# Kernel tuning notes

Measured on AMD Instinct MI355X. Metric: run time of the kernel, lower is better.

The kernel has to match this reference:

```python
import jax, jax.numpy as jnp
import numpy as np

NEG_SLOPE = 0.2  # PyG GATConv default leaky_relu slope
BN_EPS = 1e-5


def gat_conv(x_src, x_dst, src, dst, w_src, w_dst, att_src, att_dst, bias):
    """Bipartite PyG GATConv, heads=H, concat=False (mean over heads), add_self_loops=True.
    x_src: [Ns, F], x_dst: [Nd, F]; src/dst: [E] int edge index; w_*: [F, H*C]; att_*: [H, C]; bias: [C].
    """
    H, C = att_src.shape
    n_dst = x_dst.shape[0]
    hs = (x_src @ w_src).reshape(-1, H, C)            # [Ns, H, C]
    hd = (x_dst @ w_dst).reshape(-1, H, C)            # [Nd, H, C]
    a_s = (hs * att_src[None]).sum(-1)                # [Ns, H]
    a_d = (hd * att_dst[None]).sum(-1)                # [Nd, H]
    # PyG adds self loops with num_nodes = min(Ns, Nd) for bipartite inputs
    n_loop = min(x_src.shape[0], n_dst)
    loop = jnp.arange(n_loop, dtype=src.dtype)
    src = jnp.concatenate([src, loop])
    dst = jnp.concatenate([dst, loop])
    e = jax.nn.leaky_relu(a_s[src] + a_d[dst], NEG_SLOPE)           # [E+L, H]
    m = jax.ops.segment_max(e, dst, num_segments=n_dst)             # [Nd, H]
    ex = jnp.exp(e - m[dst])
    den = jax.ops.segment_sum(ex, dst, num_segments=n_dst)
    alpha = ex / (den[dst] + 1e-16)                                 # neighborhood softmax
    msg = hs[src] * alpha[:, :, None]                               # [E+L, H, C]
    out = jax.ops.segment_sum(msg, dst, num_segments=n_dst)         # [Nd, H, C]
    return out.mean(axis=1) + bias


def _forward(user_ids, ingredient_ids, recipe_x, ing_src, ing_dst, ub_src, ub_dst,
             user_table, ing_table, W_rl, b_rl, bn_gamma, bn_beta,
             g1_ws, g1_wd, g1_as, g1_ad, g1_b,
             g2_ws, g2_wd, g2_as, g2_ad, g2_b):
    # nn.Embedding(max_norm=1.0): renorm looked-up rows to L2 norm <= 1
    u = user_table[user_ids]
    un = jnp.linalg.norm(u, axis=-1, keepdims=True)
    u = u * jnp.where(un > 1.0, 1.0 / (un + 1e-7), 1.0)
    # static ingredient embedding lookup
    ing = ing_table[ingredient_ids]
    # recipe linear + BatchNorm (training-mode batch stats; dropout off = eval)
    r = recipe_x @ W_rl + b_rl
    mu = r.mean(axis=0)
    var = ((r - mu) ** 2).mean(axis=0)
    r = bn_gamma * (r - mu) * jax.lax.rsqrt(var + BN_EPS) + bn_beta
    # ingredient -> recipe GAT, residual add
    r = r + gat_conv(ing, r, ing_src, ing_dst, g1_ws, g1_wd, g1_as, g1_ad, g1_b)
    # user -> recipe GAT
    r = gat_conv(u, r, ub_src, ub_dst, g2_ws, g2_wd, g2_as, g2_ad, g2_b)
    return r


def setup_inputs() -> dict:
    key = jax.random.key(0)
    ks = jax.random.split(key, 24)
    NU, NR, NI = 50000, 100000, 20000
    D_IN, H, C = 20, 2, 128
    E1, E2 = 400000, 800000
    s = 0.05
    f32 = jnp.float32
    inp = {
        "user_ids": jax.random.randint(ks[0], (NU,), 0, NU, dtype=jnp.int32),
        "ingredient_ids": jax.random.randint(ks[1], (NI,), 0, NI, dtype=jnp.int32),
        "recipe_x": jax.random.normal(ks[2], (NR, D_IN), f32),
        "ing_src": jax.random.randint(ks[3], (E1,), 0, NI, dtype=jnp.int32),
        "ing_dst": jax.random.randint(ks[4], (E1,), 0, NR, dtype=jnp.int32),
        "ub_src": jax.random.randint(ks[5], (E2,), 0, NU, dtype=jnp.int32),
        "ub_dst": jax.random.randint(ks[6], (E2,), 0, NR, dtype=jnp.int32),
        "user_table": jax.random.normal(ks[7], (NU, C), f32) * s,
        "ing_table": jax.random.normal(ks[8], (NI, C), f32) * s,
        "W_rl": jax.random.normal(ks[9], (D_IN, C), f32) * s,
        "b_rl": jnp.zeros((C,), f32),
        "bn_gamma": jnp.ones((C,), f32),
        "bn_beta": jnp.zeros((C,), f32),
        "g1_ws": jax.random.normal(ks[10], (C, H * C), f32) * s,
        "g1_wd": jax.random.normal(ks[11], (C, H * C), f32) * s,
        "g1_as": jax.random.normal(ks[12], (H, C), f32) * s,
        "g1_ad": jax.random.normal(ks[13], (H, C), f32) * s,
        "g1_b": jnp.zeros((C,), f32),
        "g2_ws": jax.random.normal(ks[14], (C, H * C), f32) * s,
        "g2_wd": jax.random.normal(ks[15], (C, H * C), f32) * s,
        "g2_as": jax.random.normal(ks[16], (H, C), f32) * s,
        "g2_ad": jax.random.normal(ks[17], (H, C), f32) * s,
        "g2_b": jnp.zeros((C,), f32),
    }
    return inp


def reference(user_ids, ingredient_ids, recipe_x, ing_src, ing_dst, ub_src, ub_dst,
              user_table, ing_table, W_rl, b_rl, bn_gamma, bn_beta,
              g1_ws, g1_wd, g1_as, g1_ad, g1_b,
              g2_ws, g2_wd, g2_as, g2_ad, g2_b):
    return _forward(user_ids, ingredient_ids, recipe_x, ing_src, ing_dst, ub_src, ub_dst,
                    user_table, ing_table, W_rl, b_rl, bn_gamma, bn_beta,
                    g1_ws, g1_wd, g1_as, g1_ad, g1_b,
                    g2_ws, g2_wd, g2_as, g2_ad, g2_b)
```

## Files before the change

kernel.cpp:

```cpp
#include <hip/hip_runtime.h>
#include <hip/hip_bf16.h>
#include <math.h>

#define DIN 20
#define C 128
#define HC 256
#define EB2 1024
#define MAXNB 400
#define CAP 8192
#define CAPSH 13

typedef unsigned short u16;
typedef unsigned int u32;
typedef unsigned long long u64;
typedef __bf16 bf16x8 __attribute__((ext_vector_type(8)));
typedef float f32x4 __attribute__((ext_vector_type(4)));

__device__ __forceinline__ float bfbits2f(unsigned int lo16) {
    return __uint_as_float(lo16 << 16);
}
__device__ __forceinline__ u16 f2bf_rne(float f) {
    unsigned int b = __float_as_uint(f);
    return (u16)((b + 0x7FFFu + ((b >> 16) & 1u)) >> 16);
}

__device__ __forceinline__ void scan512f(u32* cnt, u32* off, u32* wsum4) {
    int t = threadIdx.x;
    int l = t & 63, w = t >> 6;
    u32 a = cnt[2 * t], b = cnt[2 * t + 1];
    u32 s = a + b;
    u32 isc = s;
    #pragma unroll
    for (int o = 1; o < 64; o <<= 1) {
        u32 n = __shfl_up(isc, o);
        if (l >= o) isc += n;
    }
    if (l == 63) wsum4[w] = isc;
    __syncthreads();
    u32 pre = 0;
    if (w > 0) pre += wsum4[0];
    if (w > 1) pre += wsum4[1];
    if (w > 2) pre += wsum4[2];
    u32 excl = pre + isc - s;
    off[2 * t] = excl;
    off[2 * t + 1] = excl + a;
    __syncthreads();
}

__device__ __forceinline__ void edge_at(int i, const int* s1, const int* d1,
    const int* s2, const int* d2, int E1, int T1, int E2, int NR,
    int& s, int& key)
{
    if (i < T1) {
        if (i < E1) { s = s1[i]; key = d1[i]; }
        else        { s = i - E1; key = i - E1; }
    } else {
        int k = i - T1;
        if (k < E2) { s = s2[k]; key = NR + d2[k]; }
        else        { s = k - E2; key = NR + (k - E2); }
    }
}

__global__ __launch_bounds__(256) void k_init(const float* __restrict__ x, int NR,
    float* __restrict__ stats, int SB, int A2B,
    const int* __restrict__ src1, const int* __restrict__ dst1,
    const int* __restrict__ src2, const int* __restrict__ dst2,
    int E1, int L1, int E2, int L2, int NB,
    u32* __restrict__ bucketFill, u64* __restrict__ pairs,
    const float* __restrict__ g2_ws, u16* __restrict__ wsp)
{
    __shared__ __align__(16) char sm[24144];
    int t = threadIdx.x;
    int bid = blockIdx.x;
    if (bid < SB) {
        float (*L)[DIN] = (float(*)[DIN])sm;
        int r = bid * 256 + t;
        if (r < NR) {
            #pragma unroll
            for (int k = 0; k < DIN; k++) L[t][k] = x[r * DIN + k];
        } else {
            #pragma unroll
            for (int k = 0; k < DIN; k++) L[t][k] = 0.f;
        }
        __syncthreads();
        if (t < 210) {
            int p = 0, q = t;
            while (q >= DIN - p) { q -= (DIN - p); p++; }
            q += p;
            float acc = 0.f;
            for (int rr = 0; rr < 256; rr++) acc += L[rr][p] * L[rr][q];
            atomicAdd(&stats[p * DIN + q], acc);
            if (p != q) atomicAdd(&stats[q * DIN + p], acc);
        } else if (t < 230) {
            int k = t - 210;
            float acc = 0.f;
            for (int rr = 0; rr < 256; rr++) acc += L[rr][k];
            atomicAdd(&stats[400 + k], acc);
        }
        return;
    }
    if (bid < SB + A2B) {
        u64* ldsE = (u64*)sm;
        u64* ldsS = ldsE + EB2;
        u32* cntA = (u32*)(ldsS + EB2);
        u32* cntB = cntA + 512;
        u32* offL = cntB + 512;
        u32* wsum4 = offL + 512;
        u32* gbase = wsum4 + 4;
        for (int i = t; i < 512; i += 256) { cntA[i] = 0; cntB[i] = 0; }
        __syncthreads();
        int T1 = E1 + L1, T = T1 + E2 + L2;
        int base = (bid - SB) * EB2;
        int nE = T - base; if (nE > EB2) nE = EB2;
        for (int j = t; j < nE; j += 256) {
            int s, key;
            edge_at(base + j, src1, dst1, src2, dst2, E1, T1, E2, NR, s, key);
            ldsE[j] = ((u64)(u32)key << 32) | (u32)s;
            atomicAdd(&cntA[key >> 9], 1u);
        }
        __syncthreads();
        scan512f(cntA, offL, wsum4);
        for (int b = t; b < NB; b += 256) {
            u32 c = cntA[b];
            gbase[b] = c ? (((u32)b << CAPSH) + atomicAdd(&bucketFill[b], c)) : 0u;
        }
        __syncthreads();
        for (int j = t; j < nE; j += 256) {
            u64 e = ldsE[j];
            u32 b = ((u32)(e >> 32)) >> 9;
            u32 r = atomicAdd(&cntB[b], 1u);
            ldsS[offL[b] + r] = e;
        }
        __syncthreads();
        for (int j = t; j < nE; j += 256) {
            u64 e = ldsS[j];
            u32 b = ((u32)(e >> 32)) >> 9;
            pairs[gbase[b] + ((u32)j - offL[b])] = e;
        }
        return;
    }
    int idx0 = ((bid - SB - A2B) * 256 + t) * 4;
    #pragma unroll
    for (int i = 0; i < 4; i++) {
        int flat = idx0 + i;
        int j = flat & 7;
        int lane = (flat >> 3) & 63;
        int kb = (flat >> 9) & 3;
        int nt = flat >> 11;
        int k = kb * 32 + (lane >> 4) * 8 + j;
        int n = nt * 16 + (lane & 15);
        wsp[flat] = f2bf_rne(g2_ws[k * HC + n]);
    }
}

__global__ __launch_bounds__(256) void k_pre(float* __restrict__ stats,
    const float* __restrict__ W,
    const float* __restrict__ gamma, const float* __restrict__ beta,
    const float* __restrict__ g1_wd, const float* __restrict__ g1_ad,
    const float* __restrict__ g2_wd, const float* __restrict__ g2_ad,
    const float* __restrict__ g1_ws, const float* __restrict__ g1_as,
    const float* __restrict__ g2_ws, const float* __restrict__ g2_as,
    const float* __restrict__ g1b, float invN)
{
    int t = threadIdx.x;
    __shared__ float Sm[420];
    __shared__ float Wm[DIN * C];
    __shared__ float vd1s[256];
    __shared__ float vd2s[256];
    __shared__ float sS[128];
    __shared__ float sSh[128];
    for (int i = t; i < 420; i += 256) Sm[i] = stats[i];
    for (int i = t; i < DIN * C; i += 256) Wm[i] = W[i];
    __syncthreads();
    if (t < C) {
        float w[DIN];
        #pragma unroll
        for (int k = 0; k < DIN; k++) w[k] = Wm[k * C + t];
        float mb = 0.f;
        #pragma unroll
        for (int k = 0; k < DIN; k++) mb += Sm[400 + k] * invN * w[k];
        float e2 = 0.f;
        for (int p = 0; p < DIN; p++) {
            float acc2 = 0.f;
            #pragma unroll
            for (int q = 0; q < DIN; q++) acc2 += Sm[p * DIN + q] * w[q];
            e2 += w[p] * acc2;
        }
        e2 *= invN;
        float var = e2 - mb * mb;
        float s = gamma[t] * rsqrtf(var + 1e-5f);
        float sh = beta[t] - s * mb;
        stats[420 + t] = s;
        stats[548 + t] = sh;
        sS[t] = s;
        sSh[t] = sh;
    }
    {
        int k = t >> 1, h = t & 1;
        const float4* wd1 = (const float4*)(g1_wd + k * HC + h * C);
        const float4* wd2 = (const float4*)(g2_wd + k * HC + h * C);
        const float4* ws1 = (const float4*)(g1_ws + k * HC + h * C);
        const float4* ws2 = (const float4*)(g2_ws + k * HC + h * C);
        const float4* ad1 = (const float4*)(g1_ad + h * C);
        const float4* ad2 = (const float4*)(g2_ad + h * C);
        const float4* as1 = (const float4*)(g1_as + h * C);
        const float4* as2 = (const float4*)(g2_as + h * C);
        float a1 = 0.f, a2 = 0.f, s1 = 0.f, s2 = 0.f;
        #pragma unroll 4
        for (int q = 0; q < 32; q++) {
            float4 x, y;
            x = wd1[q]; y = ad1[q];
            a1 += x.x * y.x + x.y * y.y + x.z * y.z + x.w * y.w;
            x = wd2[q]; y = ad2[q];
            a2 += x.x * y.x + x.y * y.y + x.z * y.z + x.w * y.w;
            x = ws1[q]; y = as1[q];
            s1 += x.x * y.x + x.y * y.y + x.z * y.z + x.w * y.w;
            x = ws2[q]; y = as2[q];
            s2 += x.x * y.x + x.y * y.y + x.z * y.z + x.w * y.w;
        }
        stats[676 + t] = a1;
        stats[932 + t] = a2;
        stats[1200 + t] = s1;
        stats[1456 + t] = s2;
        vd1s[t] = a1;
        vd2s[t] = a2;
    }
    __syncthreads();
    {
        int k = t >> 1, h = t & 1;
        const float4* ws1p = (const float4*)(g1_ws + k * HC + h * C);
        float t0 = 0.f, t1 = 0.f;
        #pragma unroll 4
        for (int q = 0; q < 32; q++) {
            float4 wv = ws1p[q];
            int c = q * 4;
            t0 += wv.x * vd2s[(c + 0) * 2 + 0] + wv.y * vd2s[(c + 1) * 2 + 0]
                + wv.z * vd2s[(c + 2) * 2 + 0] + wv.w * vd2s[(c + 3) * 2 + 0];
            t1 += wv.x * vd2s[(c + 0) * 2 + 1] + wv.y * vd2s[(c + 1) * 2 + 1]
                + wv.z * vd2s[(c + 2) * 2 + 1] + wv.w * vd2s[(c + 3) * 2 + 1];
        }
        stats[1712 + t * 2 + 0] = t0;
        stats[1712 + t * 2 + 1] = t1;
    }
    if (t < 2) {
        float cb = 0.f;
        for (int k = 0; k < C; k++) cb += g1b[k] * vd2s[k * 2 + t];
        stats[1188 + t] = cb;
    }
    if (t < 80) {
        int k = t >> 2, h4 = t & 3, h = h4 & 1;
        const float* vs = (h4 < 2) ? vd1s : vd2s;
        float acc = 0.f;
        for (int c = 0; c < C; c++) acc += sS[c] * Wm[k * C + c] * vs[c * 2 + h];
        stats[2240 + t] = acc;
    } else if (t < 84) {
        int h4 = t - 80, h = h4 & 1;
        const float* vs = (h4 < 2) ? vd1s : vd2s;
        float acc = 0.f;
        for (int c = 0; c < C; c++) acc += sSh[c] * vs[c * 2 + h];
        stats[2320 + h4] = acc;
    }
}

__global__ __launch_bounds__(256) void k_fin(const u64* __restrict__ pairs,
    const u32* __restrict__ bucketFill, int n2, int NB, int R0B, int IB,
    int* __restrict__ off2, int* __restrict__ sorted,
    const float* __restrict__ x, int NR, const float* __restrict__ stats,
    float* __restrict__ a_d, float* __restrict__ advd,
    const float* __restrict__ ing_table, const int* __restrict__ ing_ids, int NI,
    float* __restrict__ a_si, float* __restrict__ psi,
    const float* __restrict__ user_table, const int* __restrict__ user_ids, int NU,
    const u16* __restrict__ wsp, u16* __restrict__ hs16, float* __restrict__ a_su)
{
    __shared__ __align__(16) char sm[30736];
    int t = threadIdx.x;
    int bid = blockIdx.x;
    if (bid < NB) {
        u32* cntA = (u32*)sm;
        u32* cntB = cntA + 512;
        u32* offL = cntB + 512;
        u32* wsum4 = offL + 512;
        u32* ldsS = wsum4 + 4;
        int b = bid;
        u32 beg = (u32)b << CAPSH;
        u32 fill = bucketFill[b];
        u32 end = beg + fill;
        int dstBase = b << 9;
        for (int i = t; i < 512; i += 256) { cntA[i] = 0; cntB[i] = 0; }
        __syncthreads();
        for (u32 j = beg + t; j < end; j += 256) {
            u32 key = (u32)(pairs[j] >> 32);
            atomicAdd(&cntA[key - dstBase], 1u);
        }
        __syncthreads();
        scan512f(cntA, offL, wsum4);
        for (int d = t; d < 512; d += 256) {
            int gk = dstBase + d;
            if (gk < n2) {
                int s0 = (int)(beg + offL[d]);
                off2[2 * gk] = s0;
                off2[2 * gk + 1] = s0 + (int)cntA[d];
            }
        }
        bool fast = fill <= 6144u;
        __syncthreads();
        for (u32 j = beg + t; j < end; j += 256) {
            u64 e = pairs[j];
            u32 d = (u32)(e >> 32) - dstBase;
            u32 r = atomicAdd(&cntB[d], 1u);
            u32 pos = offL[d] + r;
            if (fast) ldsS[pos] = (u32)e;
            else sorted[beg + pos] = (int)(u32)e;
        }
        __syncthreads();
        if (fast) {
            for (u32 j = t; j < fill; j += 256) sorted[beg + j] = (int)ldsS[j];
        }
        return;
    }
    if (bid < NB + R0B) {
        float* fv = (float*)sm;
        if (t < 84) fv[t] = stats[2240 + t];
        __syncthreads();
        int r = (bid - NB) * 256 + t;
        if (r < NR) {
            const float4* xp = (const float4*)(x + (size_t)r * DIN);
            float4 v0 = xp[0], v1 = xp[1], v2 = xp[2], v3 = xp[3], v4 = xp[4];
            float xv[20] = {v0.x, v0.y, v0.z, v0.w, v1.x, v1.y, v1.z, v1.w,
                            v2.x, v2.y, v2.z, v2.w, v3.x, v3.y, v3.z, v3.w,
                            v4.x, v4.y, v4.z, v4.w};
            float a0 = 0.f, a1 = 0.f, b0 = 0.f, b1 = 0.f;
            #pragma unroll
            for (int k = 0; k < DIN; k++) {
                float xvk = xv[k];
                a0 += xvk * fv[k * 4 + 0];
                a1 += xvk * fv[k * 4 + 1];
                b0 += xvk * fv[k * 4 + 2];
                b1 += xvk * fv[k * 4 + 3];
            }
            ((float2*)a_d)[r]  = make_float2(a0 + fv[80], a1 + fv[81]);
            ((float2*)advd)[r] = make_float2(b0 + fv[82], b1 + fv[83]);
        }
        return;
    }
    if (bid < NB + R0B + IB) {
        float* u1s = (float*)sm;
        float* Ts  = u1s + 256;
        u1s[t] = stats[1200 + t];
        Ts[t] = stats[1712 + t];
        Ts[256 + t] = stats[1968 + t];
        __syncthreads();
        int r = t >> 3, cg = t & 7;
        int row = (bid - NB - R0B) * 32 + r;
        float as0 = 0.f, as1 = 0.f, p00 = 0.f, p01 = 0.f, p10 = 0.f, p11 = 0.f;
        if (row < NI) {
            const float* xp = ing_table + (size_t)ing_ids[row] * C + cg * 16;
            #pragma unroll
            for (int q = 0; q < 4; q++) {
                float4 v = ((const float4*)xp)[q];
                float xvv[4] = {v.x, v.y, v.z, v.w};
                #pragma unroll
                for (int jj = 0; jj < 4; jj++) {
                    int k = cg * 16 + q * 4 + jj;
                    float xx = xvv[jj];
                    as0 += xx * u1s[k * 2 + 0];
                    as1 += xx * u1s[k * 2 + 1];
                    p00 += xx * Ts[k * 4 + 0];
                    p01 += xx * Ts[k * 4 + 1];
                    p10 += xx * Ts[k * 4 + 2];
                    p11 += xx * Ts[k * 4 + 3];
                }
            }
        }
        #pragma unroll
        for (int m = 1; m <= 4; m <<= 1) {
            as0 += __shfl_xor(as0, m); as1 += __shfl_xor(as1, m);
            p00 += __shfl_xor(p00, m); p01 += __shfl_xor(p01, m);
            p10 += __shfl_xor(p10, m); p11 += __shfl_xor(p11, m);
        }
        if (cg == 0 && row < NI) {
            ((float2*)a_si)[row] = make_float2(as0, as1);
            float4 pv; pv.x = p00; pv.y = p01; pv.z = p10; pv.w = p11;
            ((float4*)psi)[row] = pv;
        }
        return;
    }
    u16* A = (u16*)sm;
    float* u2s = (float*)(sm + 8704);
    u2s[t] = stats[1456 + t];
    int rowBase = (bid - NB - R0B - IB) * 32;
    int r = t >> 3, cg = t & 7;
    int row = rowBase + r;
    float xv[16];
    if (row < NU) {
        const float* xp = user_table + (size_t)user_ids[row] * C + cg * 16;
        #pragma unroll
        for (int q = 0; q < 4; q++) {
            float4 v = ((const float4*)xp)[q];
            xv[q * 4 + 0] = v.x; xv[q * 4 + 1] = v.y;
            xv[q * 4 + 2] = v.z; xv[q * 4 + 3] = v.w;
        }
    } else {
        #pragma unroll
        for (int q = 0; q < 16; q++) xv[q] = 0.f;
    }
    float ss = 0.f;
    #pragma unroll
    for (int q = 0; q < 16; q++) ss += xv[q] * xv[q];
    #pragma unroll
    for (int m = 1; m <= 4; m <<= 1) ss += __shfl_xor(ss, m);
    float nn = sqrtf(ss);
    float f = (nn > 1.f) ? 1.f / (nn + 1e-7f) : 1.f;
    float as0 = 0.f, as1 = 0.f;
    #pragma unroll
    for (int q = 0; q < 16; q++) {
        xv[q] *= f;
        int k = cg * 16 + q;
        as0 += xv[q] * u2s[k * 2 + 0];
        as1 += xv[q] * u2s[k * 2 + 1];
    }
    #pragma unroll
    for (int m = 1; m <= 4; m <<= 1) {
        as0 += __shfl_xor(as0, m); as1 += __shfl_xor(as1, m);
    }
    if (cg == 0 && row < NU) ((float2*)a_su)[row] = make_float2(as0, as1);
    {
        union { u16 h[16]; uint4 u4[2]; } pk;
        #pragma unroll
        for (int q = 0; q < 16; q++) pk.h[q] = f2bf_rne(xv[q]);
        uint4* dst = (uint4*)&A[r * 136 + cg * 16];
        dst[0] = pk.u4[0];
        dst[1] = pk.u4[1];
    }
    __syncthreads();
    int w = t >> 6, l = t & 63;
    int m15 = l & 15, q4 = l >> 4;
    bf16x8 afrag[2][4];
    #pragma unroll
    for (int mt = 0; mt < 2; mt++)
        #pragma unroll
        for (int kb = 0; kb < 4; kb++)
            afrag[mt][kb] = *(const bf16x8*)&A[(mt * 16 + m15) * 136 + kb * 32 + q4 * 8];
    f32x4 acc[2][4];
    #pragma unroll
    for (int mt = 0; mt < 2; mt++)
        #pragma unroll
        for (int i = 0; i < 4; i++) acc[mt][i] = (f32x4){0.f, 0.f, 0.f, 0.f};
    #pragma unroll
    for (int kb = 0; kb < 4; kb++) {
        #pragma unroll
        for (int i = 0; i < 4; i++) {
            int nt = w * 4 + i;
            bf16x8 bfrag = *(const bf16x8*)&wsp[((nt * 4 + kb) * 64 + l) * 8];
            acc[0][i] = __builtin_amdgcn_mfma_f32_16x16x32_bf16(afrag[0][kb], bfrag, acc[0][i], 0, 0, 0);
            acc[1][i] = __builtin_amdgcn_mfma_f32_16x16x32_bf16(afrag[1][kb], bfrag, acc[1][i], 0, 0, 0);
        }
    }
    #pragma unroll
    for (int mt = 0; mt < 2; mt++) {
        #pragma unroll
        for (int i = 0; i < 4; i++) {
            int col = (w * 4 + i) * 16 + m15;
            #pragma unroll
            for (int rr = 0; rr < 4; rr++) {
                int rw = rowBase + mt * 16 + q4 * 4 + rr;
                if (rw < NU) hs16[(size_t)rw * HC + col] = f2bf_rne(acc[mt][i][rr]);
            }
        }
    }
}

__global__ __launch_bounds__(256) void k_agg(const int* __restrict__ off2, const int* __restrict__ sorted,
    const float* __restrict__ a_si, const float* __restrict__ psi,
    const float* __restrict__ a_d1, const float* __restrict__ advd,
    const float* __restrict__ cb,
    const float* __restrict__ a_su, const u16* __restrict__ hs16,
    const float* __restrict__ bias, int NR, float* __restrict__ out)
{
    int wave = threadIdx.x >> 6, lane = threadIdx.x & 63;
    int d = blockIdx.x * 4 + wave;
    if (d >= NR) return;
    int beg = off2[2 * d], end = off2[2 * d + 1];
    float ad0 = a_d1[d * 2 + 0], ad1 = a_d1[d * 2 + 1];
    float w0s = 0.f, w1s = 0.f, a00 = 0.f, a01 = 0.f, a10 = 0.f, a11 = 0.f;
    for (int j = beg + lane; j < end; j += 64) {
        int s = sorted[j];
        float2 as = ((const float2*)a_si)[s];
        float e0 = as.x + ad0; e0 = (e0 >= 0.f) ? e0 : 0.2f * e0;
        float e1 = as.y + ad1; e1 = (e1 >= 0.f) ? e1 : 0.2f * e1;
        float x0 = __expf(e0), x1 = __expf(e1);
        float4 p = ((const float4*)psi)[s];
        w0s += x0; w1s += x1;
        a00 += x0 * p.x; a01 += x0 * p.y;
        a10 += x1 * p.z; a11 += x1 * p.w;
    }
    #pragma unroll
    for (int o = 1; o < 64; o <<= 1) {
        w0s += __shfl_xor(w0s, o); w1s += __shfl_xor(w1s, o);
        a00 += __shfl_xor(a00, o); a01 += __shfl_xor(a01, o);
        a10 += __shfl_xor(a10, o); a11 += __shfl_xor(a11, o);
    }
    float inv0g = 1.f / (w0s + 1e-16f), inv1g = 1.f / (w1s + 1e-16f);
    float r0 = advd[d * 2 + 0] + cb[0] + 0.5f * (a00 * inv0g + a10 * inv1g);
    float r1 = advd[d * 2 + 1] + cb[1] + 0.5f * (a01 * inv0g + a11 * inv1g);
    int i2 = NR + d;
    int beg2 = off2[2 * i2], end2 = off2[2 * i2 + 1];
    int head = lane >> 5;
    int q = lane & 31;
    u32 laneoff = (u32)(head * 256 + q * 8);
    int hsel = lane & 32;
    float adh = head ? r1 : r0;
    float wsum = 0.f;
    float acc0 = 0.f, acc1 = 0.f, acc2 = 0.f, acc3 = 0.f;
    const char* hbase = (const char*)hs16;

    for (int base = beg2; base < end2; base += 32) {
        int rem = end2 - base; if (rem > 32) rem = 32;
        int j = q; if (j >= rem) j = rem - 1;
        int sp = sorted[base + j];
        u32 boff = ((u32)sp) << 9;
        float asv = a_su[sp * 2 + head];
        float ee = asv + adh; ee = (ee >= 0.f) ? ee : 0.2f * ee;
        float wcomb = __expf(ee);
        int e = 0;
        for (; e + 4 <= rem; e += 4) {
            u32 b0 = __shfl(boff, e + 0), b1 = __shfl(boff, e + 1);
            u32 b2 = __shfl(boff, e + 2), b3 = __shfl(boff, e + 3);
            uint2 g0 = *(const uint2*)(hbase + (b0 + laneoff));
            uint2 g1 = *(const uint2*)(hbase + (b1 + laneoff));
            uint2 g2 = *(const uint2*)(hbase + (b2 + laneoff));
            uint2 g3 = *(const uint2*)(hbase + (b3 + laneoff));
            float W0 = __shfl(wcomb, hsel + e + 0);
            float W1 = __shfl(wcomb, hsel + e + 1);
            float W2 = __shfl(wcomb, hsel + e + 2);
            float W3 = __shfl(wcomb, hsel + e + 3);
            wsum += (W0 + W1) + (W2 + W3);
            acc0 += W0 * bfbits2f(g0.x & 0xFFFFu);
            acc1 += W0 * __uint_as_float(g0.x & 0xFFFF0000u);
            acc2 += W0 * bfbits2f(g0.y & 0xFFFFu);
            acc3 += W0 * __uint_as_float(g0.y & 0xFFFF0000u);
            acc0 += W1 * bfbits2f(g1.x & 0xFFFFu);
            acc1 += W1 * __uint_as_float(g1.x & 0xFFFF0000u);
            acc2 += W1 * bfbits2f(g1.y & 0xFFFFu);
            acc3 += W1 * __uint_as_float(g1.y & 0xFFFF0000u);
            acc0 += W2 * bfbits2f(g2.x & 0xFFFFu);
            acc1 += W2 * __uint_as_float(g2.x & 0xFFFF0000u);
            acc2 += W2 * bfbits2f(g2.y & 0xFFFFu);
            acc3 += W2 * __uint_as_float(g2.y & 0xFFFF0000u);
            acc0 += W3 * bfbits2f(g3.x & 0xFFFFu);
            acc1 += W3 * __uint_as_float(g3.x & 0xFFFF0000u);
            acc2 += W3 * bfbits2f(g3.y & 0xFFFFu);
            acc3 += W3 * __uint_as_float(g3.y & 0xFFFF0000u);
        }
        for (; e < rem; e++) {
            u32 b0 = __shfl(boff, e);
            float W = __shfl(wcomb, hsel + e);
            uint2 g = *(const uint2*)(hbase + (b0 + laneoff));
            wsum += W;
            acc0 += W * bfbits2f(g.x & 0xFFFFu);
            acc1 += W * __uint_as_float(g.x & 0xFFFF0000u);
            acc2 += W * bfbits2f(g.y & 0xFFFFu);
            acc3 += W * __uint_as_float(g.y & 0xFFFF0000u);
        }
    }
    float inv = 1.f / (wsum + 1e-16f);
    float v0 = acc0 * inv, v1 = acc1 * inv, v2 = acc2 * inv, v3 = acc3 * inv;
    v0 = 0.5f * (v0 + __shfl_xor(v0, 32));
    v1 = 0.5f * (v1 + __shfl_xor(v1, 32));
    v2 = 0.5f * (v2 + __shfl_xor(v2, 32));
    v3 = 0.5f * (v3 + __shfl_xor(v3, 32));
    if (lane < 32) {
        float4 bb = ((const float4*)bias)[q];
        float4 o;
        o.x = v0 + bb.x; o.y = v1 + bb.y; o.z = v2 + bb.z; o.w = v3 + bb.w;
        ((float4*)(out + (size_t)d * C))[q] = o;
    }
}

extern "C" void kernel_launch(void* const* d_in, const int* in_sizes, int n_in,
                              void* d_out, int out_size, void* d_ws, size_t ws_size,
                              hipStream_t stream) {
    const int*   user_ids       = (const int*)d_in[0];
    const int*   ingredient_ids = (const int*)d_in[1];
    const float* recipe_x       = (const float*)d_in[2];
    const int*   ing_src        = (const int*)d_in[3];
    const int*   ing_dst        = (const int*)d_in[4];
    const int*   ub_src         = (const int*)d_in[5];
    const int*   ub_dst         = (const int*)d_in[6];
    const float* user_table     = (const float*)d_in[7];
    const float* ing_table      = (const float*)d_in[8];
    const float* W_rl           = (const float*)d_in[9];
    const float* bn_gamma       = (const float*)d_in[11];
    const float* bn_beta        = (const float*)d_in[12];
    const float* g1_ws          = (const float*)d_in[13];
    const float* g1_wd          = (const float*)d_in[14];
    const float* g1_as          = (const float*)d_in[15];
    const float* g1_ad          = (const float*)d_in[16];
    const float* g1_b           = (const float*)d_in[17];
    const float* g2_ws          = (const float*)d_in[18];
    const float* g2_wd          = (const float*)d_in[19];
    const float* g2_as          = (const float*)d_in[20];
    const float* g2_ad          = (const float*)d_in[21];
    const float* g2_b           = (const float*)d_in[22];

    int NU = in_sizes[0];
    int NI = in_sizes[1];
    int NR = in_sizes[2] / DIN;
    int E1 = in_sizes[3];
    int E2 = in_sizes[5];
    int Nmax = (NI > NU) ? NI : NU;
    int L1 = (NI < NR) ? NI : NR;
    int L2 = (NU < NR) ? NU : NR;
    int Etot = E1 + L1 + E2 + L2;
    int n2 = 2 * NR;
    int NB = (n2 + 511) >> 9;

    char* w = (char*)d_ws;
    u16*   hs16  = (u16*)w;    w += (size_t)Nmax * HC * 2;
    float* a_si  = (float*)w;  w += (size_t)NI * 2 * 4;
    float* a_su  = (float*)w;  w += (size_t)NU * 2 * 4;
    float* psi   = (float*)w;  w += (size_t)NI * 4 * 4;
    float* a_d   = (float*)w;  w += (size_t)NR * 2 * 4;
    float* advd  = (float*)w;  w += (size_t)NR * 2 * 4;
    float* stats = (float*)w;  w += 2432 * 4;
    u32*   bucketFill = (u32*)w; w += MAXNB * 4;
    u16*   wsp   = (u16*)w;    w += 32768 * 2;
    int*   off2  = (int*)w;    w += (size_t)(2 * n2) * 4;
    int*   sorted= (int*)w;    w += (size_t)NB * CAP * 4;
    w = (char*)(((size_t)w + 15) & ~(size_t)15);
    u64*   pairs = (u64*)w;    w += (size_t)NB * CAP * 8;

    hipMemsetAsync(stats, 0, (2432 + MAXNB) * 4, stream);

    int SB  = (NR + 255) / 256;
    int A2B = (Etot + EB2 - 1) / EB2;
    k_init<<<SB + A2B + 32, 256, 0, stream>>>(recipe_x, NR, stats, SB, A2B,
                                              ing_src, ing_dst, ub_src, ub_dst,
                                              E1, L1, E2, L2, NB,
                                              bucketFill, pairs, g2_ws, wsp);
    k_pre<<<1, 256, 0, stream>>>(stats, W_rl, bn_gamma, bn_beta,
                                 g1_wd, g1_ad, g2_wd, g2_ad,
                                 g1_ws, g1_as, g2_ws, g2_as, g1_b, 1.0f / NR);
    int R0B = (NR + 255) / 256;
    int IB  = (NI + 31) / 32;
    int HB  = (NU + 31) / 32;
    k_fin<<<NB + R0B + IB + HB, 256, 0, stream>>>(pairs, bucketFill, n2, NB, R0B, IB,
                                                  off2, sorted,
                                                  recipe_x, NR, stats, a_d, advd,
                                                  ing_table, ingredient_ids, NI, a_si, psi,
                                                  user_table, user_ids, NU,
                                                  wsp, hs16, a_su);
    k_agg<<<(NR + 3) / 4, 256, 0, stream>>>(off2, sorted, a_si, psi, a_d, advd,
                                            stats + 1188, a_su, hs16, g2_b, NR,
                                            (float*)d_out);
}
```

Baseline: 319.1 us.

## Move attention-vector projections from single-block prep kernel into parallel init blocks

The four weight-by-attention dot products, previously computed serially by the single-block k_pre kernel, now run in four extra blocks of k_init. k_pre reads the results back from stats, which shortens its serial critical path. The edge-binning chunk size is also doubled, giving fewer, larger blocks with more shared memory each, and the recipe feature row loads are vectorised to float4. The risks are lower occupancy from the larger shared allocation and less parallelism in the binning phase.

```diff
diff --git a/kernel.cpp b/kernel.cpp
--- a/kernel.cpp
+++ b/kernel.cpp
@@ -5,7 +5,7 @@
 #define DIN 20
 #define C 128
 #define HC 256
-#define EB2 1024
+#define EB2 2048
 #define MAXNB 400
 #define CAP 8192
 #define CAPSH 13
@@ -67,17 +67,26 @@
     const int* __restrict__ src2, const int* __restrict__ dst2,
     int E1, int L1, int E2, int L2, int NB,
     u32* __restrict__ bucketFill, u64* __restrict__ pairs,
-    const float* __restrict__ g2_ws, u16* __restrict__ wsp)
+    const float* __restrict__ g2_ws, u16* __restrict__ wsp,
+    const float* __restrict__ g1_wd, const float* __restrict__ g1_ad,
+    const float* __restrict__ g2_wd, const float* __restrict__ g2_ad,
+    const float* __restrict__ g1_ws, const float* __restrict__ g1_as,
+    const float* __restrict__ g2_as)
 {
-    __shared__ __align__(16) char sm[24144];
+    __shared__ __align__(16) char sm[40528];
     int t = threadIdx.x;
     int bid = blockIdx.x;
     if (bid < SB) {
         float (*L)[DIN] = (float(*)[DIN])sm;
         int r = bid * 256 + t;
         if (r < NR) {
-            #pragma unroll
-            for (int k = 0; k < DIN; k++) L[t][k] = x[r * DIN + k];
+            const float4* xp = (const float4*)(x + (size_t)r * DIN);
+            float4 v0 = xp[0], v1 = xp[1], v2 = xp[2], v3 = xp[3], v4 = xp[4];
+            L[t][0] = v0.x; L[t][1] = v0.y; L[t][2] = v0.z; L[t][3] = v0.w;
+            L[t][4] = v1.x; L[t][5] = v1.y; L[t][6] = v1.z; L[t][7] = v1.w;
+            L[t][8] = v2.x; L[t][9] = v2.y; L[t][10] = v2.z; L[t][11] = v2.w;
+            L[t][12] = v3.x; L[t][13] = v3.y; L[t][14] = v3.z; L[t][15] = v3.w;
+            L[t][16] = v4.x; L[t][17] = v4.y; L[t][18] = v4.z; L[t][19] = v4.w;
         } else {
             #pragma unroll
             for (int k = 0; k < DIN; k++) L[t][k] = 0.f;
@@ -139,28 +148,43 @@
         }
         return;
     }
-    int idx0 = ((bid - SB - A2B) * 256 + t) * 4;
-    #pragma unroll
-    for (int i = 0; i < 4; i++) {
-        int flat = idx0 + i;
-        int j = flat & 7;
-        int lane = (flat >> 3) & 63;
-        int kb = (flat >> 9) & 3;
-        int nt = flat >> 11;
-        int k = kb * 32 + (lane >> 4) * 8 + j;
-        int n = nt * 16 + (lane & 15);
-        wsp[flat] = f2bf_rne(g2_ws[k * HC + n]);
+    if (bid < SB + A2B + 32) {
+        int idx0 = ((bid - SB - A2B) * 256 + t) * 4;
+        #pragma unroll
+        for (int i = 0; i < 4; i++) {
+            int flat = idx0 + i;
+            int j = flat & 7;
+            int lane = (flat >> 3) & 63;
+            int kb = (flat >> 9) & 3;
+            int nt = flat >> 11;
+            int k = kb * 32 + (lane >> 4) * 8 + j;
+            int n = nt * 16 + (lane & 15);
+            wsp[flat] = f2bf_rne(g2_ws[k * HC + n]);
+        }
+        return;
+    }
+    int dr = bid - SB - A2B - 32;
+    const float* wm = (dr == 0) ? g1_wd : (dr == 1) ? g2_wd : (dr == 2) ? g1_ws : g2_ws;
+    const float* am = (dr == 0) ? g1_ad : (dr == 1) ? g2_ad : (dr == 2) ? g1_as : g2_as;
+    int obase = (dr == 0) ? 676 : (dr == 1) ? 932 : (dr == 2) ? 1200 : 1456;
+    {
+        int k = t >> 1, h = t & 1;
+        const float4* wp = (const float4*)(wm + k * HC + h * C);
+        const float4* ap = (const float4*)(am + h * C);
+        float acc = 0.f;
+        #pragma unroll 4
+        for (int q = 0; q < 32; q++) {
+            float4 xv = wp[q], yv = ap[q];
+            acc += xv.x * yv.x + xv.y * yv.y + xv.z * yv.z + xv.w * yv.w;
+        }
+        stats[obase + t] = acc;
     }
 }
 
 __global__ __launch_bounds__(256) void k_pre(float* __restrict__ stats,
     const float* __restrict__ W,
     const float* __restrict__ gamma, const float* __restrict__ beta,
-    const float* __restrict__ g1_wd, const float* __restrict__ g1_ad,
-    const float* __restrict__ g2_wd, const float* __restrict__ g2_ad,
-    const float* __restrict__ g1_ws, const float* __restrict__ g1_as,
-    const float* __restrict__ g2_ws, const float* __restrict__ g2_as,
-    const float* __restrict__ g1b, float invN)
+    const float* __restrict__ g1_ws, const float* __restrict__ g1b, float invN)
 {
     int t = threadIdx.x;
     __shared__ float Sm[420];
@@ -171,6 +195,8 @@
     __shared__ float sSh[128];
     for (int i = t; i < 420; i += 256) Sm[i] = stats[i];
     for (int i = t; i < DIN * C; i += 256) Wm[i] = W[i];
+    vd1s[t] = stats[676 + t];
+    vd2s[t] = stats[932 + t];
     __syncthreads();
     if (t < C) {
         float w[DIN];
@@ -195,37 +221,6 @@
         sS[t] = s;
         sSh[t] = sh;
     }
-    {
-        int k = t >> 1, h = t & 1;
-        const float4* wd1 = (const float4*)(g1_wd + k * HC + h * C);
-        const float4* wd2 = (const float4*)(g2_wd + k * HC + h * C);
-        const float4* ws1 = (const float4*)(g1_ws + k * HC + h * C);
-        const float4* ws2 = (const float4*)(g2_ws + k * HC + h * C);
-        const float4* ad1 = (const float4*)(g1_ad + h * C);
-        const float4* ad2 = (const float4*)(g2_ad + h * C);
-        const float4* as1 = (const float4*)(g1_as + h * C);
-        const float4* as2 = (const float4*)(g2_as + h * C);
-        float a1 = 0.f, a2 = 0.f, s1 = 0.f, s2 = 0.f;
-        #pragma unroll 4
-        for (int q = 0; q < 32; q++) {
-            float4 x, y;
-            x = wd1[q]; y = ad1[q];
-            a1 += x.x * y.x + x.y * y.y + x.z * y.z + x.w * y.w;
-            x = wd2[q]; y = ad2[q];
-            a2 += x.x * y.x + x.y * y.y + x.z * y.z + x.w * y.w;
-            x = ws1[q]; y = as1[q];
-            s1 += x.x * y.x + x.y * y.y + x.z * y.z + x.w * y.w;
-            x = ws2[q]; y = as2[q];
-            s2 += x.x * y.x + x.y * y.y + x.z * y.z + x.w * y.w;
-        }
-        stats[676 + t] = a1;
-        stats[932 + t] = a2;
-        stats[1200 + t] = s1;
-        stats[1456 + t] = s2;
-        vd1s[t] = a1;
-        vd2s[t] = a2;
-    }
-    __syncthreads();
     {
         int k = t >> 1, h = t & 1;
         const float4* ws1p = (const float4*)(g1_ws + k * HC + h * C);
@@ -247,6 +242,7 @@
         for (int k = 0; k < C; k++) cb += g1b[k] * vd2s[k * 2 + t];
         stats[1188 + t] = cb;
     }
+    __syncthreads();
     if (t < 80) {
         int k = t >> 2, h4 = t & 3, h = h4 & 1;
         const float* vs = (h4 < 2) ? vd1s : vd2s;
@@ -634,13 +630,14 @@
 
     int SB  = (NR + 255) / 256;
     int A2B = (Etot + EB2 - 1) / EB2;
-    k_init<<<SB + A2B + 32, 256, 0, stream>>>(recipe_x, NR, stats, SB, A2B,
+    k_init<<<SB + A2B + 32 + 4, 256, 0, stream>>>(recipe_x, NR, stats, SB, A2B,
                                               ing_src, ing_dst, ub_src, ub_dst,
                                               E1, L1, E2, L2, NB,
-                                              bucketFill, pairs, g2_ws, wsp);
+                                              bucketFill, pairs, g2_ws, wsp,
+                                              g1_wd, g1_ad, g2_wd, g2_ad,
+                                              g1_ws, g1_as, g2_as);
     k_pre<<<1, 256, 0, stream>>>(stats, W_rl, bn_gamma, bn_beta,
-                                 g1_wd, g1_ad, g2_wd, g2_ad,
-                                 g1_ws, g1_as, g2_ws, g2_as, g1_b, 1.0f / NR);
+                                 g1_ws, g1_b, 1.0f / NR);
     int R0B = (NR + 255) / 256;
     int IB  = (NI + 31) / 32;
     int HB  = (NU + 31) / 32;
```

Result: faster. 300.7 us (-5.8%).
